# Performance work log

Hardware: AMD Instinct MI355X
Metric: run time of the kernel (lower is better)

The kernel has to match this reference:

```python
import jax, jax.numpy as jnp
import numpy as np
from jax import lax

N = 20000          # num_nodes_total
N_GHOST = 2000     # nodes with mask == 0
T_IN = 8
FEAT = 16          # node_features
HID = 128          # hidden_dim
E = 320000         # edges (~avg degree 16)
D = 2              # downstream_concat_depth
ALPHA = 0.5        # alpha_boundary
FUSER_IN = FEAT * (1 + D) + 1   # 49
FUSER_H = max(32, 2 * FEAT * (1 + D))  # 96
GATE_H = max(8, FUSER_H // 2)   # 48


def _lin(k, fan_in, shape):
    b = 1.0 / np.sqrt(fan_in)
    return jax.random.uniform(k, shape, jnp.float32, -b, b)


def setup_inputs() -> dict:
    key = jax.random.key(0)
    ks = jax.random.split(key, 26)
    x = jax.random.normal(ks[0], (N, T_IN, FEAT), jnp.float32)
    src = jax.random.randint(ks[1], (E,), 0, N, jnp.int32)
    dst = jax.random.randint(ks[2], (E,), 0, N, jnp.int32)
    # guarantee every ghost node (ids [0, N_GHOST)) has an outgoing edge to a real node
    src = src.at[:N_GHOST].set(jnp.arange(N_GHOST, dtype=jnp.int32))
    dst = dst.at[:N_GHOST].set(jax.random.randint(ks[3], (N_GHOST,), N_GHOST, N, jnp.int32))
    edge_index = jnp.stack([src, dst])
    edge_attr = jax.random.uniform(ks[4], (E, 1), jnp.float32, minval=0.05, maxval=2.0)
    mask = jnp.concatenate([jnp.zeros(N_GHOST, jnp.int32), jnp.ones(N - N_GHOST, jnp.int32)])
    H3 = 3 * HID
    return dict(
        x=x, edge_attr=edge_attr,
        W_lin=_lin(ks[5], FEAT, (FEAT, HID)), b_lin=_lin(ks[6], FEAT, (HID,)),
        Wc1=_lin(ks[7], HID, (HID, HID)), bc1=jnp.zeros((HID,), jnp.float32),
        Wc2=_lin(ks[8], HID, (HID, HID)), bc2=jnp.zeros((HID,), jnp.float32),
        W_ih=_lin(ks[9], HID, (HID, H3)), b_ih=_lin(ks[10], HID, (H3,)),
        W_hh=_lin(ks[11], HID, (HID, H3)), b_hh=_lin(ks[12], HID, (H3,)),
        Wf1=_lin(ks[13], FUSER_IN, (FUSER_IN, FUSER_H)), bf1=_lin(ks[14], FUSER_IN, (FUSER_H,)),
        Wf2=_lin(ks[15], FUSER_H, (FUSER_H, FEAT)), bf2=_lin(ks[16], FUSER_H, (FEAT,)),
        Wg1=_lin(ks[17], FUSER_IN, (FUSER_IN, GATE_H)), bg1=_lin(ks[18], FUSER_IN, (GATE_H,)),
        Wg2=_lin(ks[19], GATE_H, (GATE_H, 1)), bg2=_lin(ks[20], GATE_H, (1,)),
        edge_index=edge_index, mask=mask,
    )


def _forward(x, edge_attr, W_lin, b_lin, Wc1, bc1, Wc2, bc2, W_ih, b_ih, W_hh, b_hh,
             Wf1, bf1, Wf2, bf2, Wg1, bg1, Wg2, bg2, edge_index, mask):
    src, dst = edge_index[0], edge_index[1]
    ghost_idx = jnp.nonzero(mask == 0, size=N_GHOST)[0]
    dist = jnp.maximum(edge_attr[:, 0], 1e-6)                     # [E]
    # first outgoing edge per source node (earliest edge id per src, cf. argsort trick)
    eid = jnp.arange(E, dtype=jnp.int32)
    first_eid = jax.ops.segment_min(eid, src, num_segments=N)    # int32 max where no edge
    has = first_eid < E
    safe = jnp.where(has, first_eid, 0)
    first_out = jnp.where(has, dst[safe], -1)                     # [N]
    first_dx = jnp.where(has, dist[safe], -1.0)                   # [N]
    b_idx = first_out[ghost_idx]                                  # boundary node per ghost
    dx_bnd = jnp.maximum(first_dx[ghost_idx], 1e-6)[:, None]      # [G,1]
    # D downstream hops, staying put where no outgoing edge exists
    dK, cur = [], b_idx
    for _ in range(D):
        nxt = first_out[cur]
        nxt = jnp.where(nxt < 0, cur, nxt)
        dK.append(nxt)
        cur = nxt
    # GCN symmetric normalization with self-loops (PyG gcn_norm)
    deg = jnp.zeros((N,), x.dtype).at[dst].add(1.0) + 1.0         # in-degree + self-loop
    dis = deg ** -0.5
    norm_e = (dis[src] * dis[dst])[:, None]                       # [E,1]
    norm_self = (1.0 / deg)[:, None]                              # [N,1]

    def gcn(h, W, b):
        hw = h @ W                                                # [N,HID]
        agg = jnp.zeros_like(hw).at[dst].add(hw[src] * norm_e)    # scatter-add messages
        return agg + hw * norm_self + b

    def gru(g, h):
        gi = g @ W_ih + b_ih                                      # [N,3H]
        gh = h @ W_hh + b_hh
        ir, iz, inn = jnp.split(gi, 3, axis=1)
        hr, hz, hn = jnp.split(gh, 3, axis=1)
        r = jax.nn.sigmoid(ir + hr)
        z = jax.nn.sigmoid(iz + hz)
        n = jnp.tanh(inn + r * hn)
        return (1.0 - z) * n + z * h

    def step(h, x_t):
        gf = x_t[ghost_idx]                                       # [G,F]
        feats = jnp.concatenate([gf] + [x_t[i] for i in dK] + [dx_bnd], axis=1)  # [G,FUSER_IN]
        zf = jax.nn.relu(feats @ Wf1 + bf1)
        delta = zf @ Wf2 + bf2
        gate = jax.nn.sigmoid(jax.nn.relu(feats @ Wg1 + bg1) @ Wg2 + bg2)
        x_t = x_t.at[ghost_idx].set(gf + ALPHA * delta * gate)
        g = jax.nn.relu(x_t @ W_lin + b_lin)
        g = jax.nn.relu(gcn(g, Wc1, bc1))
        g = jax.nn.relu(gcn(g, Wc2, bc2))
        return gru(g, h), None

    h0 = jnp.zeros((N, HID), x.dtype)
    h, _ = lax.scan(step, h0, jnp.swapaxes(x, 0, 1))              # scan over T_IN
    return h


def reference(x, edge_attr, W_lin, b_lin, Wc1, bc1, Wc2, bc2, W_ih, b_ih, W_hh, b_hh,
              Wf1, bf1, Wf2, bf2, Wg1, bg1, Wg2, bg2, edge_index, mask):
    return _forward(x, edge_attr, W_lin, b_lin, Wc1, bc1, Wc2, bc2, W_ih, b_ih, W_hh, b_hh,
                    Wf1, bf1, Wf2, bf2, Wg1, bg1, Wg2, bg2, edge_index, mask)
```

## Files before the change

### kernel.cpp

```cpp
#include <hip/hip_runtime.h>
#include <math.h>

#define NN 20000
#define T_IN 8
#define FEAT 16
#define HID 128
#define H3 384
#define FUSER_IN 49
#define FUSER_H 96
#define GATE_H 48
#define ALPHA 0.5f

typedef unsigned short u16;
typedef __attribute__((ext_vector_type(8))) short bf16x8_t;
typedef __attribute__((ext_vector_type(4))) float f32x4_t;

__device__ __forceinline__ float sigmoidf_(float v) { return 1.0f / (1.0f + expf(-v)); }

__device__ __forceinline__ u16 f2b(float v) {
    unsigned u = __float_as_uint(v);
    unsigned r = (u + 0x7fffu + ((u >> 16) & 1u)) >> 16;
    return (u16)r;
}
__device__ __forceinline__ float b2f(u16 u) { return __uint_as_float(((unsigned)u) << 16); }


__global__ void init_kernel(int* first_eid, int* deg_cnt, int n) {
    int i = blockIdx.x * 256 + threadIdx.x;
    if (i < n) { first_eid[i] = 0x7fffffff; deg_cnt[i] = 0; }
}

__global__ void edge_pass1(const int* __restrict__ src, const int* __restrict__ dst,
                           int* first_eid, int* deg_cnt, int e) {
    int i = blockIdx.x * 256 + threadIdx.x;
    if (i < e) {
        atomicMin(&first_eid[src[i]], i);
        atomicAdd(&deg_cnt[dst[i]], 1);
    }
}

__global__ void scan1(const int* __restrict__ cnt, int* tmp, int* bsum, int n) {
    __shared__ int buf[256];
    int tid = threadIdx.x;
    int i = blockIdx.x * 256 + tid;
    int v = (i < n) ? cnt[i] : 0;
    buf[tid] = v;
    __syncthreads();
    #pragma unroll
    for (int off = 1; off < 256; off <<= 1) {
        int t = (tid >= off) ? buf[tid - off] : 0;
        __syncthreads();
        buf[tid] += t;
        __syncthreads();
    }
    if (i < n) tmp[i] = buf[tid];
    if (tid == 255) bsum[blockIdx.x] = buf[255];
}

__global__ void scan2(int* bsum, int nb) {
    __shared__ int buf[256];
    int tid = threadIdx.x;
    int v = (tid < nb) ? bsum[tid] : 0;
    buf[tid] = v;
    __syncthreads();
    #pragma unroll
    for (int off = 1; off < 256; off <<= 1) {
        int t = (tid >= off) ? buf[tid - off] : 0;
        __syncthreads();
        buf[tid] += t;
        __syncthreads();
    }
    if (tid < nb) bsum[tid] = buf[tid];
}

__global__ void scan3(const int* __restrict__ cnt, const int* __restrict__ tmp,
                      const int* __restrict__ bsum,
                      int* row_ptr, int* fill_ptr, float* dis, float* norm_self, int n) {
    int i = blockIdx.x * 256 + threadIdx.x;
    if (i >= n) return;
    int pre = (blockIdx.x > 0) ? bsum[blockIdx.x - 1] : 0;
    int incl = tmp[i] + pre;
    int v = cnt[i];
    row_ptr[i + 1] = incl;
    fill_ptr[i] = incl - v;
    float deg = (float)v + 1.0f;
    dis[i] = 1.0f / sqrtf(deg);
    norm_self[i] = 1.0f / deg;
    if (i == 0) row_ptr[0] = 0;
}

__global__ void firsts_kernel(const int* __restrict__ first_eid, const int* __restrict__ dst,
                              const float* __restrict__ edge_attr,
                              int* first_out, float* first_dx, int n, int e) {
    int i = blockIdx.x * 256 + threadIdx.x;
    if (i >= n) return;
    int fe = first_eid[i];
    if (fe < e) {
        first_out[i] = dst[fe];
        first_dx[i] = fmaxf(edge_attr[fe], 1e-6f);
    } else {
        first_out[i] = -1;
        first_dx[i] = -1.0f;
    }
}

__global__ void edge_pass2(const int* __restrict__ src, const int* __restrict__ dst,
                           int* fill_ptr, const float* __restrict__ dis,
                           int* csr_src, float* csr_w, int e) {
    int i = blockIdx.x * 256 + threadIdx.x;
    if (i < e) {
        int d = dst[i], s = src[i];
        int pos = atomicAdd(&fill_ptr[d], 1);
        csr_src[pos] = s;
        csr_w[pos] = dis[s] * dis[d];
    }
}

__global__ void ghost_kernel(const int* __restrict__ mask, const int* __restrict__ first_out,
                             const float* __restrict__ first_dx,
                             int* d1_of, int* d2_of, float* dxb_of, int n) {
    int i = blockIdx.x * 256 + threadIdx.x;
    if (i >= n || mask[i] != 0) return;
    int b = first_out[i];
    float dxb = fmaxf(first_dx[i], 1e-6f);
    int d1, d2;
    if (b < 0) { d1 = i; d2 = i; }
    else {
        int n1 = first_out[b]; d1 = (n1 < 0) ? b : n1;
        int n2 = first_out[d1]; d2 = (n2 < 0) ? d1 : n2;
    }
    d1_of[i] = d1; d2_of[i] = d2; dxb_of[i] = dxb;
}

__global__ void zero2_kernel(float* a, int na, unsigned* b, int nb) {
    int stride = gridDim.x * 256;
    for (int i = blockIdx.x * 256 + threadIdx.x; i < na; i += stride) a[i] = 0.0f;
    for (int i = blockIdx.x * 256 + threadIdx.x; i < nb; i += stride) b[i] = 0u;
}

__global__ __launch_bounds__(256)
void wsplit_kernel(const float* __restrict__ W, u16* BT_hi, u16* BT_lo, int Ncols) {
    __shared__ float tile[32][33];
    int nb = blockIdx.x * 32;
    int kb = blockIdx.y * 32;
    int tx = threadIdx.x & 31, ty = threadIdx.x >> 5;
    #pragma unroll
    for (int r = 0; r < 32; r += 8)
        tile[ty + r][tx] = W[(size_t)(kb + ty + r) * Ncols + nb + tx];
    __syncthreads();
    #pragma unroll
    for (int r = 0; r < 32; r += 8) {
        float v = tile[tx][ty + r];
        u16 h = f2b(v);
        size_t off = (size_t)(nb + ty + r) * 128 + kb + tx;
        BT_hi[off] = h;
        BT_lo[off] = f2b(v - b2f(h));
    }
}


__global__ __launch_bounds__(128)
void fuse_lin_all(const float* __restrict__ x, const int* __restrict__ mask,
                  const int* __restrict__ d1_of, const int* __restrict__ d2_of,
                  const float* __restrict__ dxb_of,
                  const float* __restrict__ Wf1, const float* __restrict__ bf1,
                  const float* __restrict__ Wf2, const float* __restrict__ bf2,
                  const float* __restrict__ Wg1, const float* __restrict__ bg1,
                  const float* __restrict__ Wg2, const float* __restrict__ bg2,
                  const float* __restrict__ W_lin, const float* __restrict__ b_lin,
                  u16* __restrict__ g8_hi, u16* __restrict__ g8_lo, int n) {
    int i = blockIdx.x;
    int t = blockIdx.y;
    int j = threadIdx.x;
    __shared__ float feats[FUSER_IN];
    __shared__ float xf[FEAT];
    __shared__ float z1[FUSER_H];
    __shared__ float zg[GATE_H];
    __shared__ float s_gate;

    const float* xrow = &x[(i * T_IN + t) * FEAT];
    if (j < FEAT) { float v = xrow[j]; feats[j] = v; xf[j] = v; }

    bool ghost = (mask[i] == 0);
    if (ghost) {
        if (j < FEAT) {
            int d1 = d1_of[i], d2 = d2_of[i];
            feats[FEAT + j]     = x[(d1 * T_IN + t) * FEAT + j];
            feats[2 * FEAT + j] = x[(d2 * T_IN + t) * FEAT + j];
        }
        if (j == 0) feats[3 * FEAT] = dxb_of[i];
        __syncthreads();
        if (j < FUSER_H) {
            float acc = bf1[j];
            for (int k = 0; k < FUSER_IN; ++k) acc = fmaf(feats[k], Wf1[k * FUSER_H + j], acc);
            z1[j] = fmaxf(acc, 0.0f);
        }
        if (j < GATE_H) {
            float acc = bg1[j];
            for (int k = 0; k < FUSER_IN; ++k) acc = fmaf(feats[k], Wg1[k * GATE_H + j], acc);
            zg[j] = fmaxf(acc, 0.0f);
        }
        __syncthreads();
        if (j == 0) {
            float s = bg2[0];
            for (int k = 0; k < GATE_H; ++k) s = fmaf(zg[k], Wg2[k], s);
            s_gate = sigmoidf_(s);
        }
        __syncthreads();
        if (j < FEAT) {
            float acc = bf2[j];
            for (int k = 0; k < FUSER_H; ++k) acc = fmaf(z1[k], Wf2[k * FEAT + j], acc);
            xf[j] = feats[j] + ALPHA * acc * s_gate;
        }
    }
    __syncthreads();
    float acc = b_lin[j];
    #pragma unroll
    for (int k = 0; k < FEAT; ++k) acc = fmaf(xf[k], W_lin[k * HID + j], acc);
    float v = fmaxf(acc, 0.0f);
    u16 hv = f2b(v);
    size_t off = ((size_t)t * n + i) * HID + j;
    g8_hi[off] = hv;
    g8_lo[off] = f2b(v - b2f(hv));
}

__global__ __launch_bounds__(256)
void gemm_gcn_b(const u16* __restrict__ Ahi0, const u16* __restrict__ Alo0,
                const u16* __restrict__ BThi, const u16* __restrict__ BTlo,
                float* __restrict__ C0, u16* __restrict__ Cb0, int M) {
    constexpr int BM = 64;
    __shared__ u16 ldsA[2][BM * 128];
    const size_t tOff = (size_t)blockIdx.z * M * 128;
    const u16* Ahi = Ahi0 + tOff;
    const u16* Alo = Alo0 + tOff;
    float*     C   = C0 + tOff;
    u16*       Cb  = Cb0 + tOff;

    const int tid  = threadIdx.x;
    const int row0 = blockIdx.x * BM;
    constexpr int MF = BM / 32;

    #pragma unroll
    for (int it = 0; it < BM / 16; ++it) {
        int unit = tid + it * 256;
        int r = unit >> 4, s = unit & 15;
        int gr = row0 + r;
        uint4 vh = make_uint4(0, 0, 0, 0), vl = vh;
        if (gr < M) {
            vh = *reinterpret_cast<const uint4*>(&Ahi[(size_t)gr * 128 + s * 8]);
            vl = *reinterpret_cast<const uint4*>(&Alo[(size_t)gr * 128 + s * 8]);
        }
        int byte = (r * 256 + s * 16) ^ ((r & 7) << 4);
        *reinterpret_cast<uint4*>((char*)(&ldsA[0][0]) + byte) = vh;
        *reinterpret_cast<uint4*>((char*)(&ldsA[1][0]) + byte) = vl;
    }
    __syncthreads();

    const int wid  = tid >> 6;
    const int lane = tid & 63;
    const int wr = (wid >> 1) * (BM / 2);
    const int wc = (wid & 1) * 64;
    const int l15 = lane & 15;
    const int lkh = lane >> 4;

    f32x4_t acc[MF][4] = {};

    #pragma unroll
    for (int kb = 0; kb < 4; ++kb) {
        bf16x8_t ah[MF], al[MF], bh[4], bl[4];
        #pragma unroll
        for (int m = 0; m < MF; ++m) {
            int row = wr + m * 16 + l15;
            int byte = (row * 256 + kb * 64 + lkh * 16) ^ ((row & 7) << 4);
            ah[m] = *reinterpret_cast<const bf16x8_t*>((const char*)(&ldsA[0][0]) + byte);
            al[m] = *reinterpret_cast<const bf16x8_t*>((const char*)(&ldsA[1][0]) + byte);
        }
        #pragma unroll
        for (int nf = 0; nf < 4; ++nf) {
            int col = wc + nf * 16 + l15;
            size_t off = (size_t)col * 128 + kb * 32 + lkh * 8;
            bh[nf] = *reinterpret_cast<const bf16x8_t*>(&BThi[off]);
            bl[nf] = *reinterpret_cast<const bf16x8_t*>(&BTlo[off]);
        }
        #pragma unroll
        for (int m = 0; m < MF; ++m)
            #pragma unroll
            for (int nf = 0; nf < 4; ++nf) {
                acc[m][nf] = __builtin_amdgcn_mfma_f32_16x16x32_bf16(ah[m], bh[nf], acc[m][nf], 0, 0, 0);
                acc[m][nf] = __builtin_amdgcn_mfma_f32_16x16x32_bf16(ah[m], bl[nf], acc[m][nf], 0, 0, 0);
                acc[m][nf] = __builtin_amdgcn_mfma_f32_16x16x32_bf16(al[m], bh[nf], acc[m][nf], 0, 0, 0);
            }
    }

    #pragma unroll
    for (int m = 0; m < MF; ++m) {
        int rbase = row0 + wr + m * 16 + lkh * 4;
        #pragma unroll
        for (int nf = 0; nf < 4; ++nf) {
            int col = wc + nf * 16 + l15;
            #pragma unroll
            for (int r2 = 0; r2 < 4; ++r2) {
                int row = rbase + r2;
                if (row < M) {
                    float v = acc[m][nf][r2];
                    C[(size_t)row * 128 + col] = v;
                    Cb[(size_t)row * 128 + col] = f2b(v);
                }
            }
        }
    }
}

__global__ __launch_bounds__(256)
void gcn_agg_b(const float* __restrict__ hw0, const u16* __restrict__ hwb0,
               const int* __restrict__ row_ptr,
               const int* __restrict__ csr_src, const float* __restrict__ csr_w,
               const float* __restrict__ norm_self, const float* __restrict__ bias,
               u16* __restrict__ g_hi0, u16* __restrict__ g_lo0, int n) {
    int node = blockIdx.x * 8 + (threadIdx.x >> 5);
    int lane = threadIdx.x & 31;
    if (node >= n) return;
    const size_t tOff = (size_t)blockIdx.y * n * 128;
    const float* hw  = hw0 + tOff;
    const u16*   hwb = hwb0 + tOff;
    u16* g_hi = g_hi0 + tOff;
    u16* g_lo = g_lo0 + tOff;

    const float4* hw4 = reinterpret_cast<const float4*>(hw);
    float4 self = hw4[(size_t)node * 32 + lane];
    float ns = norm_self[node];
    float4 a0, a1, a2, a3;
    a0.x = self.x * ns; a0.y = self.y * ns; a0.z = self.z * ns; a0.w = self.w * ns;
    a1 = make_float4(0.f, 0.f, 0.f, 0.f); a2 = a1; a3 = a1;
    int p  = row_ptr[node];
    int p1 = row_ptr[node + 1];
    for (; p + 4 <= p1; p += 4) {
        int s0 = csr_src[p], s1 = csr_src[p + 1], s2 = csr_src[p + 2], s3 = csr_src[p + 3];
        float w0 = csr_w[p], w1 = csr_w[p + 1], w2 = csr_w[p + 2], w3 = csr_w[p + 3];
        ushort4 v0 = *reinterpret_cast<const ushort4*>(&hwb[(size_t)s0 * HID + lane * 4]);
        ushort4 v1 = *reinterpret_cast<const ushort4*>(&hwb[(size_t)s1 * HID + lane * 4]);
        ushort4 v2 = *reinterpret_cast<const ushort4*>(&hwb[(size_t)s2 * HID + lane * 4]);
        ushort4 v3 = *reinterpret_cast<const ushort4*>(&hwb[(size_t)s3 * HID + lane * 4]);
        a0.x = fmaf(b2f(v0.x), w0, a0.x); a0.y = fmaf(b2f(v0.y), w0, a0.y);
        a0.z = fmaf(b2f(v0.z), w0, a0.z); a0.w = fmaf(b2f(v0.w), w0, a0.w);
        a1.x = fmaf(b2f(v1.x), w1, a1.x); a1.y = fmaf(b2f(v1.y), w1, a1.y);
        a1.z = fmaf(b2f(v1.z), w1, a1.z); a1.w = fmaf(b2f(v1.w), w1, a1.w);
        a2.x = fmaf(b2f(v2.x), w2, a2.x); a2.y = fmaf(b2f(v2.y), w2, a2.y);
        a2.z = fmaf(b2f(v2.z), w2, a2.z); a2.w = fmaf(b2f(v2.w), w2, a2.w);
        a3.x = fmaf(b2f(v3.x), w3, a3.x); a3.y = fmaf(b2f(v3.y), w3, a3.y);
        a3.z = fmaf(b2f(v3.z), w3, a3.z); a3.w = fmaf(b2f(v3.w), w3, a3.w);
    }
    for (; p < p1; ++p) {
        int s = csr_src[p];
        float w = csr_w[p];
        ushort4 v = *reinterpret_cast<const ushort4*>(&hwb[(size_t)s * HID + lane * 4]);
        a0.x = fmaf(b2f(v.x), w, a0.x); a0.y = fmaf(b2f(v.y), w, a0.y);
        a0.z = fmaf(b2f(v.z), w, a0.z); a0.w = fmaf(b2f(v.w), w, a0.w);
    }
    float4 b4 = reinterpret_cast<const float4*>(bias)[lane];
    float ox = fmaxf(a0.x + a1.x + a2.x + a3.x + b4.x, 0.0f);
    float oy = fmaxf(a0.y + a1.y + a2.y + a3.y + b4.y, 0.0f);
    float oz = fmaxf(a0.z + a1.z + a2.z + a3.z + b4.z, 0.0f);
    float ow = fmaxf(a0.w + a1.w + a2.w + a3.w + b4.w, 0.0f);
    ushort4 hv, lv;
    hv.x = f2b(ox); lv.x = f2b(ox - b2f(hv.x));
    hv.y = f2b(oy); lv.y = f2b(oy - b2f(hv.y));
    hv.z = f2b(oz); lv.z = f2b(oz - b2f(hv.z));
    hv.w = f2b(ow); lv.w = f2b(ow - b2f(hv.w));
    *reinterpret_cast<ushort4*>(&g_hi[(size_t)node * HID + lane * 4]) = hv;
    *reinterpret_cast<ushort4*>(&g_lo[(size_t)node * HID + lane * 4]) = lv;
}


__global__ __launch_bounds__(256)
void gemm_gru(const u16* __restrict__ Ahi1, const u16* __restrict__ Alo1,
              const u16* __restrict__ BThi1, const u16* __restrict__ BTlo1,
              float* __restrict__ C1,
              const u16* __restrict__ Ahi2, const u16* __restrict__ Alo2,
              const u16* __restrict__ BThi2, const u16* __restrict__ BTlo2,
              float* __restrict__ C2,
              int M, int Ncols) {
    constexpr int BM = 128;
    __shared__ u16 ldsA[2][BM * 128];
    const u16* Ahi  = blockIdx.z ? Ahi2  : Ahi1;
    const u16* Alo  = blockIdx.z ? Alo2  : Alo1;
    const u16* BThi = blockIdx.z ? BThi2 : BThi1;
    const u16* BTlo = blockIdx.z ? BTlo2 : BTlo1;
    float*     C    = blockIdx.z ? C2    : C1;

    const int tid  = threadIdx.x;
    const int row0 = blockIdx.x * BM;
    const int col0 = blockIdx.y * 128;
    constexpr int MF = BM / 32;

    #pragma unroll
    for (int it = 0; it < BM / 16; ++it) {
        int unit = tid + it * 256;
        int r = unit >> 4, s = unit & 15;
        int gr = row0 + r;
        uint4 vh = make_uint4(0, 0, 0, 0), vl = vh;
        if (gr < M) {
            vh = *reinterpret_cast<const uint4*>(&Ahi[(size_t)gr * 128 + s * 8]);
            vl = *reinterpret_cast<const uint4*>(&Alo[(size_t)gr * 128 + s * 8]);
        }
        int byte = (r * 256 + s * 16) ^ ((r & 7) << 4);
        *reinterpret_cast<uint4*>((char*)(&ldsA[0][0]) + byte) = vh;
        *reinterpret_cast<uint4*>((char*)(&ldsA[1][0]) + byte) = vl;
    }
    __syncthreads();

    const int wid  = tid >> 6;
    const int lane = tid & 63;
    const int wr = (wid >> 1) * (BM / 2);
    const int wc = (wid & 1) * 64;
    const int l15 = lane & 15;
    const int lkh = lane >> 4;

    f32x4_t acc[MF][4] = {};

    #pragma unroll
    for (int kb = 0; kb < 4; ++kb) {
        bf16x8_t ah[MF], al[MF], bh[4], bl[4];
        #pragma unroll
        for (int m = 0; m < MF; ++m) {
            int row = wr + m * 16 + l15;
            int byte = (row * 256 + kb * 64 + lkh * 16) ^ ((row & 7) << 4);
            ah[m] = *reinterpret_cast<const bf16x8_t*>((const char*)(&ldsA[0][0]) + byte);
            al[m] = *reinterpret_cast<const bf16x8_t*>((const char*)(&ldsA[1][0]) + byte);
        }
        #pragma unroll
        for (int nf = 0; nf < 4; ++nf) {
            int col = col0 + wc + nf * 16 + l15;
            size_t off = (size_t)col * 128 + kb * 32 + lkh * 8;
            bh[nf] = *reinterpret_cast<const bf16x8_t*>(&BThi[off]);
            bl[nf] = *reinterpret_cast<const bf16x8_t*>(&BTlo[off]);
        }
        #pragma unroll
        for (int m = 0; m < MF; ++m)
            #pragma unroll
            for (int nf = 0; nf < 4; ++nf) {
                acc[m][nf] = __builtin_amdgcn_mfma_f32_16x16x32_bf16(ah[m], bh[nf], acc[m][nf], 0, 0, 0);
                acc[m][nf] = __builtin_amdgcn_mfma_f32_16x16x32_bf16(ah[m], bl[nf], acc[m][nf], 0, 0, 0);
                acc[m][nf] = __builtin_amdgcn_mfma_f32_16x16x32_bf16(al[m], bh[nf], acc[m][nf], 0, 0, 0);
            }
    }

    #pragma unroll
    for (int m = 0; m < MF; ++m) {
        int rbase = row0 + wr + m * 16 + lkh * 4;
        #pragma unroll
        for (int nf = 0; nf < 4; ++nf) {
            int col = col0 + wc + nf * 16 + l15;
            #pragma unroll
            for (int r2 = 0; r2 < 4; ++r2) {
                int row = rbase + r2;
                if (row < M) C[(size_t)row * Ncols + col] = acc[m][nf][r2];
            }
        }
    }
}

__global__ __launch_bounds__(256)
void gru_kernel(const float* __restrict__ gi, const float* __restrict__ gh,
                const float* __restrict__ b_ih, const float* __restrict__ b_hh,
                float* __restrict__ h, u16* __restrict__ h_hi, u16* __restrict__ h_lo, int n) {
    int idx = blockIdx.x * 256 + threadIdx.x;
    if (idx >= n * 32) return;
    int row = idx >> 5, q = idx & 31;
    const float4* gi4 = reinterpret_cast<const float4*>(gi + (size_t)row * H3);
    const float4* gh4 = reinterpret_cast<const float4*>(gh + (size_t)row * H3);
    const float4* bi4 = reinterpret_cast<const float4*>(b_ih);
    const float4* bh4 = reinterpret_cast<const float4*>(b_hh);
    float4 vir = gi4[q], viz = gi4[32 + q], vin = gi4[64 + q];
    float4 vhr = gh4[q], vhz = gh4[32 + q], vhn = gh4[64 + q];
    float4 bir = bi4[q], biz = bi4[32 + q], bin_ = bi4[64 + q];
    float4 bhr = bh4[q], bhz = bh4[32 + q], bhn = bh4[64 + q];
    float4* h4 = reinterpret_cast<float4*>(h);
    float4 hv = h4[idx];
    float4 o;
    {
        float r = sigmoidf_((vir.x + bir.x) + (vhr.x + bhr.x));
        float z = sigmoidf_((viz.x + biz.x) + (vhz.x + bhz.x));
        float nn2 = tanhf((vin.x + bin_.x) + r * (vhn.x + bhn.x));
        o.x = (1.0f - z) * nn2 + z * hv.x;
    }
    {
        float r = sigmoidf_((vir.y + bir.y) + (vhr.y + bhr.y));
        float z = sigmoidf_((viz.y + biz.y) + (vhz.y + bhz.y));
        float nn2 = tanhf((vin.y + bin_.y) + r * (vhn.y + bhn.y));
        o.y = (1.0f - z) * nn2 + z * hv.y;
    }
    {
        float r = sigmoidf_((vir.z + bir.z) + (vhr.z + bhr.z));
        float z = sigmoidf_((viz.z + biz.z) + (vhz.z + bhz.z));
        float nn2 = tanhf((vin.z + bin_.z) + r * (vhn.z + bhn.z));
        o.z = (1.0f - z) * nn2 + z * hv.z;
    }
    {
        float r = sigmoidf_((vir.w + bir.w) + (vhr.w + bhr.w));
        float z = sigmoidf_((viz.w + biz.w) + (vhz.w + bhz.w));
        float nn2 = tanhf((vin.w + bin_.w) + r * (vhn.w + bhn.w));
        o.w = (1.0f - z) * nn2 + z * hv.w;
    }
    h4[idx] = o;
    ushort4 hvv, lvv;
    hvv.x = f2b(o.x); lvv.x = f2b(o.x - b2f(hvv.x));
    hvv.y = f2b(o.y); lvv.y = f2b(o.y - b2f(hvv.y));
    hvv.z = f2b(o.z); lvv.z = f2b(o.z - b2f(hvv.z));
    hvv.w = f2b(o.w); lvv.w = f2b(o.w - b2f(hvv.w));
    *reinterpret_cast<ushort4*>(&h_hi[(size_t)row * HID + q * 4]) = hvv;
    *reinterpret_cast<ushort4*>(&h_lo[(size_t)row * HID + q * 4]) = lvv;
}


extern "C" void kernel_launch(void* const* d_in, const int* in_sizes, int n_in,
                              void* d_out, int out_size, void* d_ws, size_t ws_size,
                              hipStream_t stream) {
    const float* x        = (const float*)d_in[0];
    const float* edge_attr= (const float*)d_in[1];
    const float* W_lin    = (const float*)d_in[2];
    const float* b_lin    = (const float*)d_in[3];
    const float* Wc1      = (const float*)d_in[4];
    const float* bc1      = (const float*)d_in[5];
    const float* Wc2      = (const float*)d_in[6];
    const float* bc2      = (const float*)d_in[7];
    const float* W_ih     = (const float*)d_in[8];
    const float* b_ih     = (const float*)d_in[9];
    const float* W_hh     = (const float*)d_in[10];
    const float* b_hh     = (const float*)d_in[11];
    const float* Wf1      = (const float*)d_in[12];
    const float* bf1      = (const float*)d_in[13];
    const float* Wf2      = (const float*)d_in[14];
    const float* bf2      = (const float*)d_in[15];
    const float* Wg1      = (const float*)d_in[16];
    const float* bg1      = (const float*)d_in[17];
    const float* Wg2      = (const float*)d_in[18];
    const float* bg2      = (const float*)d_in[19];
    const int*   edge_index = (const int*)d_in[20];
    const int*   mask     = (const int*)d_in[21];

    const int n = in_sizes[21];
    const int e = in_sizes[1];
    const int* src = edge_index;
    const int* dst = edge_index + e;
    float* h = (float*)d_out;

    char* w = (char*)d_ws;
    auto alloc = [&](size_t bytes) -> char* {
        char* p = w;
        w += (bytes + 255) & ~(size_t)255;
        return p;
    };
    int*   first_eid = (int*)  alloc((size_t)n * 4);
    int*   deg_cnt   = (int*)  alloc((size_t)n * 4);
    int*   row_ptr   = (int*)  alloc((size_t)(n + 1) * 4);
    int*   fill_ptr  = (int*)  alloc((size_t)n * 4);
    int*   tmp_scan  = (int*)  alloc((size_t)n * 4);
    int*   bsum      = (int*)  alloc((size_t)256 * 4);
    float* dis       = (float*)alloc((size_t)n * 4);
    float* norm_self = (float*)alloc((size_t)n * 4);
    int*   first_out = (int*)  alloc((size_t)n * 4);
    float* first_dx  = (float*)alloc((size_t)n * 4);
    int*   d1_of     = (int*)  alloc((size_t)n * 4);
    int*   d2_of     = (int*)  alloc((size_t)n * 4);
    float* dxb_of    = (float*)alloc((size_t)n * 4);
    int*   csr_src   = (int*)  alloc((size_t)e * 4);
    float* csr_w     = (float*)alloc((size_t)e * 4);
    u16* Wc1T_hi = (u16*)alloc((size_t)HID * 128 * 2);
    u16* Wc1T_lo = (u16*)alloc((size_t)HID * 128 * 2);
    u16* Wc2T_hi = (u16*)alloc((size_t)HID * 128 * 2);
    u16* Wc2T_lo = (u16*)alloc((size_t)HID * 128 * 2);
    u16* WihT_hi = (u16*)alloc((size_t)H3 * 128 * 2);
    u16* WihT_lo = (u16*)alloc((size_t)H3 * 128 * 2);
    u16* WhhT_hi = (u16*)alloc((size_t)H3 * 128 * 2);
    u16* WhhT_lo = (u16*)alloc((size_t)H3 * 128 * 2);
    u16*   g8_hi = (u16*)  alloc((size_t)T_IN * n * HID * 2);
    u16*   g8_lo = (u16*)  alloc((size_t)T_IN * n * HID * 2);
    float* bufH  = (float*)alloc((size_t)T_IN * n * HID * 4);
    u16*   bufHb = (u16*)  alloc((size_t)T_IN * n * HID * 2);
    u16*   h_hi  = (u16*)  alloc((size_t)n * HID * 2);
    u16*   h_lo  = (u16*)  alloc((size_t)n * HID * 2);

    float* bufGi = bufH;
    float* bufGh = bufH + (size_t)n * H3;

    const int TPB = 256;
    const int nb = (n + 255) / 256;
    dim3 gN(nb), gE((e + TPB - 1) / TPB);

    init_kernel<<<gN, TPB, 0, stream>>>(first_eid, deg_cnt, n);
    edge_pass1<<<gE, TPB, 0, stream>>>(src, dst, first_eid, deg_cnt, e);
    scan1<<<gN, TPB, 0, stream>>>(deg_cnt, tmp_scan, bsum, n);
    scan2<<<1, TPB, 0, stream>>>(bsum, nb);
    scan3<<<gN, TPB, 0, stream>>>(deg_cnt, tmp_scan, bsum, row_ptr, fill_ptr, dis, norm_self, n);
    firsts_kernel<<<gN, TPB, 0, stream>>>(first_eid, dst, edge_attr, first_out, first_dx, n, e);
    edge_pass2<<<gE, TPB, 0, stream>>>(src, dst, fill_ptr, dis, csr_src, csr_w, e);
    ghost_kernel<<<gN, TPB, 0, stream>>>(mask, first_out, first_dx, d1_of, d2_of, dxb_of, n);
    wsplit_kernel<<<dim3(HID / 32, 4), TPB, 0, stream>>>(Wc1, Wc1T_hi, Wc1T_lo, HID);
    wsplit_kernel<<<dim3(HID / 32, 4), TPB, 0, stream>>>(Wc2, Wc2T_hi, Wc2T_lo, HID);
    wsplit_kernel<<<dim3(H3 / 32, 4), TPB, 0, stream>>>(W_ih, WihT_hi, WihT_lo, H3);
    wsplit_kernel<<<dim3(H3 / 32, 4), TPB, 0, stream>>>(W_hh, WhhT_hi, WhhT_lo, H3);

    zero2_kernel<<<2048, TPB, 0, stream>>>(h, n * HID, (unsigned*)h_hi, n * HID);

    dim3 grid_fuse(n, T_IN);
    dim3 grid_gcn((n + 63) / 64, 1, T_IN);
    dim3 grid_agg((n + 7) / 8, T_IN);

    fuse_lin_all<<<grid_fuse, 128, 0, stream>>>(x, mask, d1_of, d2_of, dxb_of,
                                                Wf1, bf1, Wf2, bf2, Wg1, bg1, Wg2, bg2,
                                                W_lin, b_lin, g8_hi, g8_lo, n);
    gemm_gcn_b<<<grid_gcn, 256, 0, stream>>>(g8_hi, g8_lo, Wc1T_hi, Wc1T_lo, bufH, bufHb, n);
    gcn_agg_b<<<grid_agg, 256, 0, stream>>>(bufH, bufHb, row_ptr, csr_src, csr_w,
                                            norm_self, bc1, g8_hi, g8_lo, n);
    gemm_gcn_b<<<grid_gcn, 256, 0, stream>>>(g8_hi, g8_lo, Wc2T_hi, Wc2T_lo, bufH, bufHb, n);
    gcn_agg_b<<<grid_agg, 256, 0, stream>>>(bufH, bufHb, row_ptr, csr_src, csr_w,
                                            norm_self, bc2, g8_hi, g8_lo, n);

    dim3 grid_gru((n + 127) / 128, 3, 2);
    for (int t = 0; t < T_IN; ++t) {
        const u16* Gt_hi = g8_hi + (size_t)t * n * HID;
        const u16* Gt_lo = g8_lo + (size_t)t * n * HID;
        gemm_gru<<<grid_gru, 256, 0, stream>>>(
            Gt_hi, Gt_lo, WihT_hi, WihT_lo, bufGi,
            h_hi, h_lo, WhhT_hi, WhhT_lo, bufGh, n, H3);
        gru_kernel<<<(n * 32 + TPB - 1) / TPB, TPB, 0, stream>>>(bufGi, bufGh, b_ih, b_hh,
                                                                 h, h_hi, h_lo, n);
    }
}
```

Measured before the change: 945.1 us.

## Split ghost fuser from lin, drop fp32 GCN output, interleave agg blocks

Builds a compact ghost list so the fuser MLP runs only for ghost nodes. A separate grid-stride lin_all kernel computes the input projection for all nodes, using weights held in shared memory. The GCN GEMM no longer writes an fp32 copy of its output, and aggregation reads the self term from bf16, which cuts write and read traffic but lowers self-term precision. Aggregation blocks are interleaved across timesteps so nodes that share neighbor rows run close together. The fuser still launches n×T blocks, and most of them exit early.

Result: no change. 938.0 us (-0.7%).

```diff
diff --git a/kernel.cpp b/kernel.cpp
--- a/kernel.cpp
+++ b/kernel.cpp
@@ -25,9 +25,10 @@
 __device__ __forceinline__ float b2f(u16 u) { return __uint_as_float(((unsigned)u) << 16); }
 
 
-__global__ void init_kernel(int* first_eid, int* deg_cnt, int n) {
+__global__ void init_kernel(int* first_eid, int* deg_cnt, int* gcount, int n) {
     int i = blockIdx.x * 256 + threadIdx.x;
     if (i < n) { first_eid[i] = 0x7fffffff; deg_cnt[i] = 0; }
+    if (i == 0) *gcount = 0;
 }
 
 __global__ void edge_pass1(const int* __restrict__ src, const int* __restrict__ dst,
@@ -118,9 +119,14 @@
 
 __global__ void ghost_kernel(const int* __restrict__ mask, const int* __restrict__ first_out,
                              const float* __restrict__ first_dx,
-                             int* d1_of, int* d2_of, float* dxb_of, int n) {
+                             int* d1_of, int* d2_of, float* dxb_of,
+                             int* ghost_list, int* ghost_pos, int* gcount, int n) {
     int i = blockIdx.x * 256 + threadIdx.x;
-    if (i >= n || mask[i] != 0) return;
+    if (i >= n) return;
+    if (mask[i] != 0) { ghost_pos[i] = -1; return; }
+    int pos = atomicAdd(gcount, 1);
+    ghost_list[pos] = i;
+    ghost_pos[i] = pos;
     int b = first_out[i];
     float dxb = fmaxf(first_dx[i], 1e-6f);
     int d1, d2;
@@ -160,80 +166,98 @@
 
 
 __global__ __launch_bounds__(128)
-void fuse_lin_all(const float* __restrict__ x, const int* __restrict__ mask,
-                  const int* __restrict__ d1_of, const int* __restrict__ d2_of,
-                  const float* __restrict__ dxb_of,
-                  const float* __restrict__ Wf1, const float* __restrict__ bf1,
-                  const float* __restrict__ Wf2, const float* __restrict__ bf2,
-                  const float* __restrict__ Wg1, const float* __restrict__ bg1,
-                  const float* __restrict__ Wg2, const float* __restrict__ bg2,
-                  const float* __restrict__ W_lin, const float* __restrict__ b_lin,
-                  u16* __restrict__ g8_hi, u16* __restrict__ g8_lo, int n) {
-    int i = blockIdx.x;
+void fuse_ghost(const float* __restrict__ x,
+                const int* __restrict__ ghost_list, const int* __restrict__ gcount,
+                const int* __restrict__ d1_of, const int* __restrict__ d2_of,
+                const float* __restrict__ dxb_of,
+                const float* __restrict__ Wf1, const float* __restrict__ bf1,
+                const float* __restrict__ Wf2, const float* __restrict__ bf2,
+                const float* __restrict__ Wg1, const float* __restrict__ bg1,
+                const float* __restrict__ Wg2, const float* __restrict__ bg2,
+                float* __restrict__ xf_buf) {
+    int slot = blockIdx.x;
+    if (slot >= *gcount) return;
     int t = blockIdx.y;
+    int i = ghost_list[slot];
     int j = threadIdx.x;
     __shared__ float feats[FUSER_IN];
-    __shared__ float xf[FEAT];
     __shared__ float z1[FUSER_H];
     __shared__ float zg[GATE_H];
     __shared__ float s_gate;
 
-    const float* xrow = &x[(i * T_IN + t) * FEAT];
-    if (j < FEAT) { float v = xrow[j]; feats[j] = v; xf[j] = v; }
-
-    bool ghost = (mask[i] == 0);
-    if (ghost) {
-        if (j < FEAT) {
-            int d1 = d1_of[i], d2 = d2_of[i];
-            feats[FEAT + j]     = x[(d1 * T_IN + t) * FEAT + j];
-            feats[2 * FEAT + j] = x[(d2 * T_IN + t) * FEAT + j];
-        }
-        if (j == 0) feats[3 * FEAT] = dxb_of[i];
-        __syncthreads();
-        if (j < FUSER_H) {
-            float acc = bf1[j];
-            for (int k = 0; k < FUSER_IN; ++k) acc = fmaf(feats[k], Wf1[k * FUSER_H + j], acc);
-            z1[j] = fmaxf(acc, 0.0f);
-        }
-        if (j < GATE_H) {
-            float acc = bg1[j];
-            for (int k = 0; k < FUSER_IN; ++k) acc = fmaf(feats[k], Wg1[k * GATE_H + j], acc);
-            zg[j] = fmaxf(acc, 0.0f);
-        }
-        __syncthreads();
-        if (j == 0) {
-            float s = bg2[0];
-            for (int k = 0; k < GATE_H; ++k) s = fmaf(zg[k], Wg2[k], s);
-            s_gate = sigmoidf_(s);
-        }
-        __syncthreads();
-        if (j < FEAT) {
-            float acc = bf2[j];
-            for (int k = 0; k < FUSER_H; ++k) acc = fmaf(z1[k], Wf2[k * FEAT + j], acc);
-            xf[j] = feats[j] + ALPHA * acc * s_gate;
-        }
-    }
-    __syncthreads();
-    float acc = b_lin[j];
-    #pragma unroll
-    for (int k = 0; k < FEAT; ++k) acc = fmaf(xf[k], W_lin[k * HID + j], acc);
-    float v = fmaxf(acc, 0.0f);
-    u16 hv = f2b(v);
-    size_t off = ((size_t)t * n + i) * HID + j;
-    g8_hi[off] = hv;
-    g8_lo[off] = f2b(v - b2f(hv));
+    if (j < FEAT) {
+        int d1 = d1_of[i], d2 = d2_of[i];
+        feats[j]            = x[((size_t)i * T_IN + t) * FEAT + j];
+        feats[FEAT + j]     = x[((size_t)d1 * T_IN + t) * FEAT + j];
+        feats[2 * FEAT + j] = x[((size_t)d2 * T_IN + t) * FEAT + j];
+    }
+    if (j == 0) feats[3 * FEAT] = dxb_of[i];
+    __syncthreads();
+    if (j < FUSER_H) {
+        float acc = bf1[j];
+        for (int k = 0; k < FUSER_IN; ++k) acc = fmaf(feats[k], Wf1[k * FUSER_H + j], acc);
+        z1[j] = fmaxf(acc, 0.0f);
+    }
+    if (j < GATE_H) {
+        float acc = bg1[j];
+        for (int k = 0; k < FUSER_IN; ++k) acc = fmaf(feats[k], Wg1[k * GATE_H + j], acc);
+        zg[j] = fmaxf(acc, 0.0f);
+    }
+    __syncthreads();
+    if (j == 0) {
+        float s = bg2[0];
+        for (int k = 0; k < GATE_H; ++k) s = fmaf(zg[k], Wg2[k], s);
+        s_gate = sigmoidf_(s);
+    }
+    __syncthreads();
+    if (j < FEAT) {
+        float acc = bf2[j];
+        for (int k = 0; k < FUSER_H; ++k) acc = fmaf(z1[k], Wf2[k * FEAT + j], acc);
+        xf_buf[((size_t)slot * T_IN + t) * FEAT + j] = feats[j] + ALPHA * acc * s_gate;
+    }
+}
+
+__global__ __launch_bounds__(256)
+void lin_all(const float* __restrict__ x, const float* __restrict__ xf_buf,
+             const int* __restrict__ ghost_pos,
+             const float* __restrict__ W_lin, const float* __restrict__ b_lin,
+             u16* __restrict__ g8_hi, u16* __restrict__ g8_lo, int n, int total) {
+    __shared__ float Wl[FEAT][HID];
+    __shared__ float bl[HID];
+    #pragma unroll
+    for (int k8 = 0; k8 < 8; ++k8) {
+        int idx = threadIdx.x + k8 * 256;
+        Wl[idx >> 7][idx & 127] = W_lin[idx];
+    }
+    if (threadIdx.x < HID) bl[threadIdx.x] = b_lin[threadIdx.x];
+    __syncthreads();
+    int j = threadIdx.x & 127;
+    for (int pair = blockIdx.x * 2 + (threadIdx.x >> 7); pair < total; pair += gridDim.x * 2) {
+        int node = pair % n;
+        int t = pair / n;
+        int gp = ghost_pos[node];
+        const float* xr = (gp >= 0) ? &xf_buf[((size_t)gp * T_IN + t) * FEAT]
+                                    : &x[((size_t)node * T_IN + t) * FEAT];
+        float acc = bl[j];
+        #pragma unroll
+        for (int k = 0; k < FEAT; ++k) acc = fmaf(xr[k], Wl[k][j], acc);
+        float v = fmaxf(acc, 0.0f);
+        u16 hv = f2b(v);
+        size_t off = (size_t)pair * HID + j;
+        g8_hi[off] = hv;
+        g8_lo[off] = f2b(v - b2f(hv));
+    }
 }
 
 __global__ __launch_bounds__(256)
 void gemm_gcn_b(const u16* __restrict__ Ahi0, const u16* __restrict__ Alo0,
                 const u16* __restrict__ BThi, const u16* __restrict__ BTlo,
-                float* __restrict__ C0, u16* __restrict__ Cb0, int M) {
+                u16* __restrict__ Cb0, int M) {
     constexpr int BM = 64;
     __shared__ u16 ldsA[2][BM * 128];
     const size_t tOff = (size_t)blockIdx.z * M * 128;
     const u16* Ahi = Ahi0 + tOff;
     const u16* Alo = Alo0 + tOff;
-    float*     C   = C0 + tOff;
     u16*       Cb  = Cb0 + tOff;
 
     const int tid  = threadIdx.x;
@@ -301,36 +325,32 @@
             #pragma unroll
             for (int r2 = 0; r2 < 4; ++r2) {
                 int row = rbase + r2;
-                if (row < M) {
-                    float v = acc[m][nf][r2];
-                    C[(size_t)row * 128 + col] = v;
-                    Cb[(size_t)row * 128 + col] = f2b(v);
-                }
+                if (row < M) Cb[(size_t)row * 128 + col] = f2b(acc[m][nf][r2]);
             }
         }
     }
 }
 
 __global__ __launch_bounds__(256)
-void gcn_agg_b(const float* __restrict__ hw0, const u16* __restrict__ hwb0,
+void gcn_agg_b(const u16* __restrict__ hwb0,
                const int* __restrict__ row_ptr,
                const int* __restrict__ csr_src, const float* __restrict__ csr_w,
                const float* __restrict__ norm_self, const float* __restrict__ bias,
                u16* __restrict__ g_hi0, u16* __restrict__ g_lo0, int n) {
-    int node = blockIdx.x * 8 + (threadIdx.x >> 5);
+    int t   = blockIdx.x & 7;
+    int blk = blockIdx.x >> 3;
+    int node = blk * 8 + (threadIdx.x >> 5);
     int lane = threadIdx.x & 31;
     if (node >= n) return;
-    const size_t tOff = (size_t)blockIdx.y * n * 128;
-    const float* hw  = hw0 + tOff;
-    const u16*   hwb = hwb0 + tOff;
+    const size_t tOff = (size_t)t * n * 128;
+    const u16* hwb = hwb0 + tOff;
     u16* g_hi = g_hi0 + tOff;
     u16* g_lo = g_lo0 + tOff;
 
-    const float4* hw4 = reinterpret_cast<const float4*>(hw);
-    float4 self = hw4[(size_t)node * 32 + lane];
+    ushort4 sv = *reinterpret_cast<const ushort4*>(&hwb[(size_t)node * HID + lane * 4]);
     float ns = norm_self[node];
     float4 a0, a1, a2, a3;
-    a0.x = self.x * ns; a0.y = self.y * ns; a0.z = self.z * ns; a0.w = self.w * ns;
+    a0.x = b2f(sv.x) * ns; a0.y = b2f(sv.y) * ns; a0.z = b2f(sv.z) * ns; a0.w = b2f(sv.w) * ns;
     a1 = make_float4(0.f, 0.f, 0.f, 0.f); a2 = a1; a3 = a1;
     int p  = row_ptr[node];
     int p1 = row_ptr[node + 1];
@@ -564,6 +584,9 @@
     int*   d1_of     = (int*)  alloc((size_t)n * 4);
     int*   d2_of     = (int*)  alloc((size_t)n * 4);
     float* dxb_of    = (float*)alloc((size_t)n * 4);
+    int*   ghost_list= (int*)  alloc((size_t)n * 4);
+    int*   ghost_pos = (int*)  alloc((size_t)n * 4);
+    int*   gcount    = (int*)  alloc(256);
     int*   csr_src   = (int*)  alloc((size_t)e * 4);
     float* csr_w     = (float*)alloc((size_t)e * 4);
     u16* Wc1T_hi = (u16*)alloc((size_t)HID * 128 * 2);
@@ -576,26 +599,26 @@
     u16* WhhT_lo = (u16*)alloc((size_t)H3 * 128 * 2);
     u16*   g8_hi = (u16*)  alloc((size_t)T_IN * n * HID * 2);
     u16*   g8_lo = (u16*)  alloc((size_t)T_IN * n * HID * 2);
-    float* bufH  = (float*)alloc((size_t)T_IN * n * HID * 4);
     u16*   bufHb = (u16*)  alloc((size_t)T_IN * n * HID * 2);
+    float* bufGi = (float*)alloc((size_t)n * H3 * 4);
+    float* bufGh = (float*)alloc((size_t)n * H3 * 4);
+    float* xf_buf= (float*)alloc((size_t)n * T_IN * FEAT * 4);
     u16*   h_hi  = (u16*)  alloc((size_t)n * HID * 2);
     u16*   h_lo  = (u16*)  alloc((size_t)n * HID * 2);
-
-    float* bufGi = bufH;
-    float* bufGh = bufH + (size_t)n * H3;
 
     const int TPB = 256;
     const int nb = (n + 255) / 256;
     dim3 gN(nb), gE((e + TPB - 1) / TPB);
 
-    init_kernel<<<gN, TPB, 0, stream>>>(first_eid, deg_cnt, n);
+    init_kernel<<<gN, TPB, 0, stream>>>(first_eid, deg_cnt, gcount, n);
     edge_pass1<<<gE, TPB, 0, stream>>>(src, dst, first_eid, deg_cnt, e);
     scan1<<<gN, TPB, 0, stream>>>(deg_cnt, tmp_scan, bsum, n);
     scan2<<<1, TPB, 0, stream>>>(bsum, nb);
     scan3<<<gN, TPB, 0, stream>>>(deg_cnt, tmp_scan, bsum, row_ptr, fill_ptr, dis, norm_self, n);
     firsts_kernel<<<gN, TPB, 0, stream>>>(first_eid, dst, edge_attr, first_out, first_dx, n, e);
     edge_pass2<<<gE, TPB, 0, stream>>>(src, dst, fill_ptr, dis, csr_src, csr_w, e);
-    ghost_kernel<<<gN, TPB, 0, stream>>>(mask, first_out, first_dx, d1_of, d2_of, dxb_of, n);
+    ghost_kernel<<<gN, TPB, 0, stream>>>(mask, first_out, first_dx, d1_of, d2_of, dxb_of,
+                                         ghost_list, ghost_pos, gcount, n);
     wsplit_kernel<<<dim3(HID / 32, 4), TPB, 0, stream>>>(Wc1, Wc1T_hi, Wc1T_lo, HID);
     wsplit_kernel<<<dim3(HID / 32, 4), TPB, 0, stream>>>(Wc2, Wc2T_hi, Wc2T_lo, HID);
     wsplit_kernel<<<dim3(H3 / 32, 4), TPB, 0, stream>>>(W_ih, WihT_hi, WihT_lo, H3);
@@ -603,19 +626,19 @@
 
     zero2_kernel<<<2048, TPB, 0, stream>>>(h, n * HID, (unsigned*)h_hi, n * HID);
 
-    dim3 grid_fuse(n, T_IN);
+    fuse_ghost<<<dim3(n, T_IN), 128, 0, stream>>>(x, ghost_list, gcount, d1_of, d2_of, dxb_of,
+                                                  Wf1, bf1, Wf2, bf2, Wg1, bg1, Wg2, bg2,
+                                                  xf_buf);
+    lin_all<<<2048, 256, 0, stream>>>(x, xf_buf, ghost_pos, W_lin, b_lin,
+                                      g8_hi, g8_lo, n, n * T_IN);
     dim3 grid_gcn((n + 63) / 64, 1, T_IN);
-    dim3 grid_agg((n + 7) / 8, T_IN);
-
-    fuse_lin_all<<<grid_fuse, 128, 0, stream>>>(x, mask, d1_of, d2_of, dxb_of,
-                                                Wf1, bf1, Wf2, bf2, Wg1, bg1, Wg2, bg2,
-                                                W_lin, b_lin, g8_hi, g8_lo, n);
-    gemm_gcn_b<<<grid_gcn, 256, 0, stream>>>(g8_hi, g8_lo, Wc1T_hi, Wc1T_lo, bufH, bufHb, n);
-    gcn_agg_b<<<grid_agg, 256, 0, stream>>>(bufH, bufHb, row_ptr, csr_src, csr_w,
-                                            norm_self, bc1, g8_hi, g8_lo, n);
-    gemm_gcn_b<<<grid_gcn, 256, 0, stream>>>(g8_hi, g8_lo, Wc2T_hi, Wc2T_lo, bufH, bufHb, n);
-    gcn_agg_b<<<grid_agg, 256, 0, stream>>>(bufH, bufHb, row_ptr, csr_src, csr_w,
-                                            norm_self, bc2, g8_hi, g8_lo, n);
+    const int agg_blocks = ((n + 7) / 8) * T_IN;
+    gemm_gcn_b<<<grid_gcn, 256, 0, stream>>>(g8_hi, g8_lo, Wc1T_hi, Wc1T_lo, bufHb, n);
+    gcn_agg_b<<<agg_blocks, 256, 0, stream>>>(bufHb, row_ptr, csr_src, csr_w,
+                                              norm_self, bc1, g8_hi, g8_lo, n);
+    gemm_gcn_b<<<grid_gcn, 256, 0, stream>>>(g8_hi, g8_lo, Wc2T_hi, Wc2T_lo, bufHb, n);
+    gcn_agg_b<<<agg_blocks, 256, 0, stream>>>(bufHb, row_ptr, csr_src, csr_w,
+                                              norm_self, bc2, g8_hi, g8_lo, n);
 
     dim3 grid_gru((n + 127) / 128, 3, 2);
     for (int t = 0; t < T_IN; ++t) {
```
